# Performance work log

Measured on AMD Instinct MI355X. Metric: run time of the kernel, lower is better.

## Reference

```python
import jax, jax.numpy as jnp
import numpy as np

N_NODES = 100000
N_EDGES = 1600000
IN_DIM = 128
HID = 128
OUT_DIM = 64
N_GRAPHS = 128
BN_EPS = 1e-5


def _bn(h, gamma, beta):
    # training-mode BatchNorm1d: biased batch statistics over the node axis
    mu = jnp.mean(h, axis=0)
    var = jnp.mean(jnp.square(h - mu), axis=0)
    return gamma * (h - mu) * jax.lax.rsqrt(var + BN_EPS) + beta


def _gcn(h, W, b, src, dst, norm, n):
    # GCNConv: x @ W, symmetric-normalized scatter-add aggregation, + bias
    h = h @ W                                   # [N, F_out]
    msg = h[src] * norm[:, None]                # gather per edge (incl. self-loops)
    agg = jax.ops.segment_sum(msg, dst, num_segments=n)
    return agg + b


def setup_inputs() -> dict:
    key = jax.random.key(0)
    ks = jax.random.split(key, 24)
    x = jax.random.normal(ks[0], (N_NODES, IN_DIM), dtype=jnp.float32)
    edge_index = jax.random.randint(ks[1], (2, N_EDGES), 0, N_NODES, dtype=jnp.int32)
    batch = jnp.sort(jax.random.randint(ks[2], (N_NODES,), 0, N_GRAPHS, dtype=jnp.int32))
    dims = [(IN_DIM, HID), (HID, HID), (HID, HID), (HID, OUT_DIM)]
    inp = {"x": x, "edge_index": edge_index, "batch": batch}
    for i, (fi, fo) in enumerate(dims):
        inp[f"W{i}"] = jax.random.normal(ks[3 + i], (fi, fo), dtype=jnp.float32) / np.sqrt(fi)
        inp[f"b{i}"] = jnp.zeros((fo,), dtype=jnp.float32)
        inp[f"g{i}"] = jnp.ones((fo,), dtype=jnp.float32)
        inp[f"be{i}"] = jnp.zeros((fo,), dtype=jnp.float32)
    inp["skip_weight"] = jnp.float32(0.1)
    return inp


def reference(x, edge_index, batch,
              W0, b0, g0, be0, W1, b1, g1, be1,
              W2, b2, g2, be2, W3, b3, g3, be3, skip_weight):
    n = x.shape[0]
    loops = jnp.arange(n, dtype=edge_index.dtype)
    src = jnp.concatenate([edge_index[0], loops])
    dst = jnp.concatenate([edge_index[1], loops])
    deg = jax.ops.segment_sum(jnp.ones_like(src, dtype=x.dtype), dst, num_segments=n)
    dinv = jax.lax.rsqrt(jnp.maximum(deg, 1.0))  # deg >= 1 due to self-loops
    norm = dinv[src] * dinv[dst]

    # layer 0 (dropout is identity in eval reference)
    h = jax.nn.relu(_bn(_gcn(x, W0, b0, src, dst, norm, n), g0, be0))
    # middle layers with skip connections
    for W, b, g, be in ((W1, b1, g1, be1), (W2, b2, g2, be2)):
        h_prev = h
        h = jax.nn.relu(_bn(_gcn(h, W, b, src, dst, norm, n), g, be))
        h = h + skip_weight * h_prev
    # final layer, no relu
    h = _bn(_gcn(h, W3, b3, src, dst, norm, n), g3, be3)

    # global mean pool over graphs
    sums = jax.ops.segment_sum(h, batch, num_segments=N_GRAPHS)
    cnts = jax.ops.segment_sum(jnp.ones((n,), dtype=h.dtype), batch, num_segments=N_GRAPHS)
    return sums / jnp.maximum(cnts, 1.0)[:, None]
```

## Files before the change

### kernel.cpp

```cpp
#include <hip/hip_runtime.h>


typedef unsigned short u16;
typedef unsigned int u32;
typedef __attribute__((ext_vector_type(8))) short bf16x8;
typedef __attribute__((ext_vector_type(4))) float f32x4;

__device__ __forceinline__ float bflo(u32 u) { return __uint_as_float(u << 16); }
__device__ __forceinline__ float bfhi(u32 u) { return __uint_as_float(u & 0xffff0000u); }
__device__ __forceinline__ u16 f2bf(float f) {
    u32 u = __float_as_uint(f);
    u32 r = u + 0x7fffu + ((u >> 16) & 1u);
    return (u16)(r >> 16);
}
__device__ __forceinline__ u32 pack2(float a, float b) {
    return (u32)f2bf(a) | ((u32)f2bf(b) << 16);
}


__global__ void k_deg(const int* __restrict__ edst, int E, int* __restrict__ deg) {
    int e = blockIdx.x * blockDim.x + threadIdx.x;
    if (e < E) atomicAdd(&deg[edst[e]], 1);
}

__global__ void k_dinv(const int* __restrict__ deg, int n, float* __restrict__ dinv) {
    int i = blockIdx.x * blockDim.x + threadIdx.x;
    if (i < n) {
        int c = deg[i] + 1;
        dinv[i] = rsqrtf((float)c);
    }
}

__global__ void k_bsum(const int* __restrict__ deg, int n, int* __restrict__ bsum) {
    __shared__ int sd[256];
    int base = blockIdx.x * 1024;
    int end = base + 1024; if (end > n) end = n;
    int s = 0;
    for (int i = base + threadIdx.x; i < end; i += 256) s += deg[i] + 1;
    sd[threadIdx.x] = s;
    __syncthreads();
    for (int off = 128; off > 0; off >>= 1) {
        if (threadIdx.x < off) sd[threadIdx.x] += sd[threadIdx.x + off];
        __syncthreads();
    }
    if (threadIdx.x == 0) bsum[blockIdx.x] = sd[0];
}

__global__ void k_scanb(int* __restrict__ bsum, int B) {
    int run = 0;
    for (int i = 0; i < B; ++i) { int v = bsum[i]; bsum[i] = run; run += v; }
}

__global__ void k_offs(const int* __restrict__ deg, int n, const int* __restrict__ bsum,
                       int* __restrict__ offs) {
    __shared__ int sd[256];
    int base = blockIdx.x * 1024;
    int carry = bsum[blockIdx.x];
    for (int tile = 0; tile < 4; ++tile) {
        int i = base + tile * 256 + threadIdx.x;
        int v = (i < n) ? (deg[i] + 1) : 0;
        sd[threadIdx.x] = v;
        __syncthreads();
        int x = v;
        for (int off = 1; off < 256; off <<= 1) {
            int y = (threadIdx.x >= off) ? sd[threadIdx.x - off] : 0;
            __syncthreads();
            x += y;
            sd[threadIdx.x] = x;
            __syncthreads();
        }
        if (i < n) offs[i] = carry + x - v;
        if (i == n - 1) offs[n] = carry + x;
        carry += sd[255];
        __syncthreads();
    }
}

__global__ void k_fill_edges(const int* __restrict__ esrc, const int* __restrict__ edst, int E,
                             const float* __restrict__ dinv, const int* __restrict__ offs,
                             int* __restrict__ cursor, uint2* __restrict__ csre) {
    int e = blockIdx.x * blockDim.x + threadIdx.x;
    if (e < E) {
        int s = esrc[e], d = edst[e];
        int slot = offs[d] + atomicAdd(&cursor[d], 1);
        csre[slot] = make_uint2((u32)s, __float_as_uint(dinv[s] * dinv[d]));
    }
}

__global__ void k_fill_self(int n, const float* __restrict__ dinv, const int* __restrict__ offs,
                            int* __restrict__ cursor, uint2* __restrict__ csre) {
    int i = blockIdx.x * blockDim.x + threadIdx.x;
    if (i < n) {
        int slot = offs[i] + atomicAdd(&cursor[i], 1);
        csre[slot] = make_uint2((u32)i, __float_as_uint(dinv[i] * dinv[i]));
    }
}

__global__ void k_gcnt_bs(const int* __restrict__ batch, int n, int* __restrict__ gcnt) {
    int g = threadIdx.x;
    if (g < 128) {
        int lo0 = 0, hi0 = n;
        while (lo0 < hi0) { int m = (lo0 + hi0) >> 1; if (batch[m] < g) lo0 = m + 1; else hi0 = m; }
        int lo1 = lo0, hi1 = n;
        while (lo1 < hi1) { int m = (lo1 + hi1) >> 1; if (batch[m] < g + 1) lo1 = m + 1; else hi1 = m; }
        gcnt[g] = lo1 - lo0;
    }
}


template <int FOUT>
__global__ void k_wt(const float* __restrict__ W, u16* __restrict__ Wt) {
    __shared__ u16 l[128 * (FOUT + 8)];
    for (int i = threadIdx.x; i < 128 * FOUT; i += 256) {
        int k = i / FOUT, nn = i % FOUT;
        l[k * (FOUT + 8) + nn] = f2bf(W[i]);
    }
    __syncthreads();
    for (int i = threadIdx.x; i < 128 * FOUT; i += 256) {
        int nn = i >> 7, k = i & 127;
        Wt[nn * 128 + k] = l[k * (FOUT + 8) + nn];
    }
}


template <int FOUT, int MODE, bool STOREH>
__global__ __launch_bounds__(256) void k_gemm_mfma(const void* __restrict__ Ap,
                                                   const u16* __restrict__ hprev,
                                                   const float* __restrict__ coef,
                                                   const float* __restrict__ swp,
                                                   const u16* __restrict__ Wt,
                                                   u16* __restrict__ hout,
                                                   u16* __restrict__ O, int n) {
    constexpr int NT = FOUT / 16;
    const int lane = threadIdx.x & 63;
    const int wave = threadIdx.x >> 6;
    const int fr = lane & 15;
    const int fq = lane >> 4;
    const int rowbase = blockIdx.x * 64 + wave * 16;
    const int arow = rowbase + fr;
    const bool aok = arow < n;
    const float* af = (const float*)Ap + (size_t)arow * 128 + fq * 8;
    const u16* hp = (MODE == 3) ? hprev + (size_t)arow * 128 + fq * 8 : nullptr;
    const u16* wp = Wt + fr * 128 + fq * 8;
    float sw = 0.f;
    if constexpr (MODE == 3) sw = *swp;

    f32x4 acc[NT];
#pragma unroll
    for (int t = 0; t < NT; ++t)
#pragma unroll
        for (int q = 0; q < 4; ++q) acc[t][q] = 0.f;

#pragma unroll
    for (int kk = 0; kk < 4; ++kk) {
        bf16x8 a;
#pragma unroll
        for (int q = 0; q < 8; ++q) a[q] = 0;
        if (aok) {
            if constexpr (MODE == 1) {
                const float4 x0 = *(const float4*)(af + kk * 32);
                const float4 x1 = *(const float4*)(af + kk * 32 + 4);
                a[0] = (short)f2bf(x0.x); a[1] = (short)f2bf(x0.y);
                a[2] = (short)f2bf(x0.z); a[3] = (short)f2bf(x0.w);
                a[4] = (short)f2bf(x1.x); a[5] = (short)f2bf(x1.y);
                a[6] = (short)f2bf(x1.z); a[7] = (short)f2bf(x1.w);
            } else {
                const int k0 = kk * 32 + fq * 8;
                const float4 v0 = *(const float4*)(af + kk * 32);
                const float4 v1 = *(const float4*)(af + kk * 32 + 4);
                const float4 sc0 = *(const float4*)&coef[k0];
                const float4 sc1 = *(const float4*)&coef[k0 + 4];
                const float4 sh0 = *(const float4*)&coef[128 + k0];
                const float4 sh1 = *(const float4*)&coef[128 + k0 + 4];
                float r[8];
                r[0] = fmaxf(fmaf(v0.x, sc0.x, sh0.x), 0.f);
                r[1] = fmaxf(fmaf(v0.y, sc0.y, sh0.y), 0.f);
                r[2] = fmaxf(fmaf(v0.z, sc0.z, sh0.z), 0.f);
                r[3] = fmaxf(fmaf(v0.w, sc0.w, sh0.w), 0.f);
                r[4] = fmaxf(fmaf(v1.x, sc1.x, sh1.x), 0.f);
                r[5] = fmaxf(fmaf(v1.y, sc1.y, sh1.y), 0.f);
                r[6] = fmaxf(fmaf(v1.z, sc1.z, sh1.z), 0.f);
                r[7] = fmaxf(fmaf(v1.w, sc1.w, sh1.w), 0.f);
                if constexpr (MODE == 3) {
                    const uint4 pv = *(const uint4*)(hp + kk * 32);
                    r[0] = fmaf(sw, bflo(pv.x), r[0]); r[1] = fmaf(sw, bfhi(pv.x), r[1]);
                    r[2] = fmaf(sw, bflo(pv.y), r[2]); r[3] = fmaf(sw, bfhi(pv.y), r[3]);
                    r[4] = fmaf(sw, bflo(pv.z), r[4]); r[5] = fmaf(sw, bfhi(pv.z), r[5]);
                    r[6] = fmaf(sw, bflo(pv.w), r[6]); r[7] = fmaf(sw, bfhi(pv.w), r[7]);
                }
                uint4 o;
                o.x = pack2(r[0], r[1]);
                o.y = pack2(r[2], r[3]);
                o.z = pack2(r[4], r[5]);
                o.w = pack2(r[6], r[7]);
                a = *(const bf16x8*)&o;
                if constexpr (STOREH)
                    *(uint4*)&hout[(size_t)arow * 128 + k0] = o;
            }
        }
#pragma unroll
        for (int t = 0; t < NT; ++t) {
            bf16x8 b = *(const bf16x8*)(wp + t * 16 * 128 + kk * 32);
            acc[t] = __builtin_amdgcn_mfma_f32_16x16x32_bf16(a, b, acc[t], 0, 0, 0);
        }
    }
#pragma unroll
    for (int i = 0; i < 4; ++i) {
        const int row = rowbase + fq * 4 + i;
        if (row < n) {
#pragma unroll
            for (int t = 0; t < NT; ++t)
                O[(size_t)row * FOUT + t * 16 + fr] = f2bf(acc[t][i]);
        }
    }
}


template <int F>
__global__ __launch_bounds__(256) void k_agg(const u16* __restrict__ hW,
                                             const uint2* __restrict__ csre,
                                             const int* __restrict__ offs,
                                             float* __restrict__ agg, int n) {
    constexpr int TPN = F / 8;
    constexpr int NPB = 256 / TPN;
    const int lane = threadIdx.x % TPN;
    const int sub = threadIdx.x / TPN;
    const int fbase = lane * 8;

    for (int node = blockIdx.x * NPB + sub; node < n; node += gridDim.x * NPB) {
        const int beg = offs[node];
        const int end = offs[node + 1];
        float4 b0 = make_float4(0.f, 0.f, 0.f, 0.f);
        float4 b1 = make_float4(0.f, 0.f, 0.f, 0.f);
        float4 c0 = make_float4(0.f, 0.f, 0.f, 0.f);
        float4 c1 = make_float4(0.f, 0.f, 0.f, 0.f);
        int j = beg;
        for (; j + 8 <= end; j += 8) {
            uint2 ei[8];
#pragma unroll
            for (int q = 0; q < 8; ++q) ei[q] = csre[j + q];
            uint4 v[8];
#pragma unroll
            for (int q = 0; q < 8; ++q)
                v[q] = *(const uint4*)&hW[(size_t)ei[q].x * F + fbase];
#pragma unroll
            for (int q = 0; q < 8; ++q) {
                const float w = __uint_as_float(ei[q].y);
                if (q & 1) {
                    c0.x = fmaf(bflo(v[q].x), w, c0.x); c0.y = fmaf(bfhi(v[q].x), w, c0.y);
                    c0.z = fmaf(bflo(v[q].y), w, c0.z); c0.w = fmaf(bfhi(v[q].y), w, c0.w);
                    c1.x = fmaf(bflo(v[q].z), w, c1.x); c1.y = fmaf(bfhi(v[q].z), w, c1.y);
                    c1.z = fmaf(bflo(v[q].w), w, c1.z); c1.w = fmaf(bfhi(v[q].w), w, c1.w);
                } else {
                    b0.x = fmaf(bflo(v[q].x), w, b0.x); b0.y = fmaf(bfhi(v[q].x), w, b0.y);
                    b0.z = fmaf(bflo(v[q].y), w, b0.z); b0.w = fmaf(bfhi(v[q].y), w, b0.w);
                    b1.x = fmaf(bflo(v[q].z), w, b1.x); b1.y = fmaf(bfhi(v[q].z), w, b1.y);
                    b1.z = fmaf(bflo(v[q].w), w, b1.z); b1.w = fmaf(bfhi(v[q].w), w, b1.w);
                }
            }
        }
        for (; j < end; ++j) {
            const uint2 e0 = csre[j];
            const float w = __uint_as_float(e0.y);
            const uint4 v0 = *(const uint4*)&hW[(size_t)e0.x * F + fbase];
            b0.x = fmaf(bflo(v0.x), w, b0.x); b0.y = fmaf(bfhi(v0.x), w, b0.y);
            b0.z = fmaf(bflo(v0.y), w, b0.z); b0.w = fmaf(bfhi(v0.y), w, b0.w);
            b1.x = fmaf(bflo(v0.z), w, b1.x); b1.y = fmaf(bfhi(v0.z), w, b1.y);
            b1.z = fmaf(bflo(v0.w), w, b1.z); b1.w = fmaf(bfhi(v0.w), w, b1.w);
        }
        b0.x += c0.x; b0.y += c0.y; b0.z += c0.z; b0.w += c0.w;
        b1.x += c1.x; b1.y += c1.y; b1.z += c1.z; b1.w += c1.w;
        __builtin_nontemporal_store(*(const f32x4*)&b0,
                                    (f32x4*)&agg[(size_t)node * F + fbase]);
        __builtin_nontemporal_store(*(const f32x4*)&b1,
                                    (f32x4*)&agg[(size_t)node * F + fbase + 4]);
    }
}


template <int F>
__global__ __launch_bounds__(256) void k_stats(const float* __restrict__ aggf,
                                               float* __restrict__ stats,
                                               int* __restrict__ ticket,
                                               const float* __restrict__ g,
                                               const float* __restrict__ be,
                                               float* __restrict__ coef,
                                               float inv_n, int n8) {
    constexpr int TPR = F / 8;
    const int tid0 = blockIdx.x * 256 + threadIdx.x;
    float s[8], q[8];
#pragma unroll
    for (int k = 0; k < 8; ++k) { s[k] = 0.f; q[k] = 0.f; }
    for (int i = tid0; i < n8; i += gridDim.x * 256) {
        const float4 v0 = *(const float4*)&aggf[(size_t)i * 8];
        const float4 v1 = *(const float4*)&aggf[(size_t)i * 8 + 4];
        s[0] += v0.x; s[1] += v0.y; s[2] += v0.z; s[3] += v0.w;
        s[4] += v1.x; s[5] += v1.y; s[6] += v1.z; s[7] += v1.w;
        q[0] = fmaf(v0.x, v0.x, q[0]); q[1] = fmaf(v0.y, v0.y, q[1]);
        q[2] = fmaf(v0.z, v0.z, q[2]); q[3] = fmaf(v0.w, v0.w, q[3]);
        q[4] = fmaf(v1.x, v1.x, q[4]); q[5] = fmaf(v1.y, v1.y, q[5]);
        q[6] = fmaf(v1.z, v1.z, q[6]); q[7] = fmaf(v1.w, v1.w, q[7]);
    }
#pragma unroll
    for (int m = TPR; m < 64; m <<= 1) {
#pragma unroll
        for (int k = 0; k < 8; ++k) {
            s[k] += __shfl_xor(s[k], m);
            q[k] += __shfl_xor(q[k], m);
        }
    }
    __shared__ float sred[2][4][TPR * 8];
    const int w = threadIdx.x >> 6;
    const int l64 = threadIdx.x & 63;
    if (l64 < TPR) {
#pragma unroll
        for (int k = 0; k < 8; ++k) {
            sred[0][w][l64 * 8 + k] = s[k];
            sred[1][w][l64 * 8 + k] = q[k];
        }
    }
    __syncthreads();
    if (threadIdx.x < TPR * 8) {
        float a = sred[0][0][threadIdx.x] + sred[0][1][threadIdx.x] +
                  sred[0][2][threadIdx.x] + sred[0][3][threadIdx.x];
        float b = sred[1][0][threadIdx.x] + sred[1][1][threadIdx.x] +
                  sred[1][2][threadIdx.x] + sred[1][3][threadIdx.x];
        const int ff = threadIdx.x & (F - 1);
        atomicAdd(&stats[ff], a);
        atomicAdd(&stats[F + ff], b);
    }
    __threadfence();
    __shared__ int last;
    if (threadIdx.x == 0) last = (atomicAdd(ticket, 1) == (int)gridDim.x - 1) ? 1 : 0;
    __syncthreads();
    if (last) {
        if (threadIdx.x < F) {
            const int f = threadIdx.x;
            float sum = atomicAdd(&stats[f], 0.f);
            float ssq = atomicAdd(&stats[F + f], 0.f);
            float mean = sum * inv_n;
            float var = fmaxf(ssq * inv_n - mean * mean, 0.f);
            float sc = g[f] * rsqrtf(var + 1e-5f);
            coef[f] = sc;
            coef[F + f] = be[f] - mean * sc;
        }
    }
}


__global__ __launch_bounds__(256) void k_bnpool(const float* __restrict__ C,
                                                const int* __restrict__ batch,
                                                const float* __restrict__ coef,
                                                float* __restrict__ out, int n,
                                                int chunk) {
    __shared__ float pool[128 * 64];
    for (int i = threadIdx.x; i < 128 * 64; i += 256) pool[i] = 0.f;
    __syncthreads();
    const int f = threadIdx.x & 63;
    const int sub = threadIdx.x >> 6;
    const float sc = coef[f];
    const float sh = coef[64 + f];
    const int lo = blockIdx.x * chunk;
    int hi = lo + chunk; if (hi > n) hi = n;
    for (int node = lo + sub; node < hi; node += 4) {
        float v = fmaf(sc, C[(size_t)node * 64 + f], sh);
        int g = batch[node];
        atomicAdd(&pool[g * 64 + f], v);
    }
    __syncthreads();
    for (int i = threadIdx.x; i < 128 * 64; i += 256) {
        float v = pool[i];
        if (v != 0.f) atomicAdd(&out[i], v);
    }
}

__global__ void k_div(float* __restrict__ out, const int* __restrict__ gcnt, int total) {
    int i = blockIdx.x * blockDim.x + threadIdx.x;
    if (i < total) {
        int g = i >> 6;
        int c = gcnt[g];
        if (c < 1) c = 1;
        out[i] = out[i] / (float)c;
    }
}


static inline size_t align256(size_t x) { return (x + 255) & ~(size_t)255; }

extern "C" void kernel_launch(void* const* d_in, const int* in_sizes, int n_in,
                              void* d_out, int out_size, void* d_ws, size_t ws_size,
                              hipStream_t stream) {
    const float* x    = (const float*)d_in[0];
    const int* ei     = (const int*)d_in[1];
    const int* batch  = (const int*)d_in[2];
    const float* W0   = (const float*)d_in[3];
    const float* g0   = (const float*)d_in[5];
    const float* be0  = (const float*)d_in[6];
    const float* W1   = (const float*)d_in[7];
    const float* g1   = (const float*)d_in[9];
    const float* be1  = (const float*)d_in[10];
    const float* W2   = (const float*)d_in[11];
    const float* g2   = (const float*)d_in[13];
    const float* be2  = (const float*)d_in[14];
    const float* W3   = (const float*)d_in[15];
    const float* g3   = (const float*)d_in[17];
    const float* be3  = (const float*)d_in[18];
    const float* swp  = (const float*)d_in[19];

    const int N = in_sizes[0] / 128;
    const int E = in_sizes[1] / 2;
    const int T = E + N;
    const int* esrc = ei;
    const int* edst = ei + E;

    char* p = (char*)d_ws;
    auto carve = [&](size_t bytes) -> char* {
        char* r = p;
        p += align256(bytes);
        return r;
    };
    int*   deg    = (int*)carve((size_t)N * 4);
    float* dinv   = (float*)carve((size_t)N * 4);
    int*   offs   = (int*)carve((size_t)(N + 1) * 4);
    int*   cursor = (int*)carve((size_t)N * 4);
    int*   bsum   = (int*)carve(256 * 4);
    uint2* csre   = (uint2*)carve((size_t)T * 8);
    float* stats  = (float*)carve(4 * 256 * 4);
    float* coef   = (float*)carve(4 * 256 * 4);
    int*   ticket = (int*)carve(4 * 4);
    int*   gcnt   = (int*)carve(128 * 4);
    u16*   Wt0    = (u16*)carve(128 * 128 * 2);
    u16*   Wt1    = (u16*)carve(128 * 128 * 2);
    u16*   Wt2    = (u16*)carve(128 * 128 * 2);
    u16*   Wt3    = (u16*)carve(64 * 128 * 2);
    u16*   h0     = (u16*)carve((size_t)N * 128 * 2);
    u16*   h1     = (u16*)carve((size_t)N * 128 * 2);
    u16*   hWb    = (u16*)carve((size_t)N * 128 * 2);
    float* aggf   = (float*)carve((size_t)N * 128 * 4);

    hipMemsetAsync(deg, 0, (size_t)N * 4, stream);
    hipMemsetAsync(cursor, 0, (size_t)N * 4, stream);
    hipMemsetAsync(stats, 0, 4 * 256 * 4, stream);
    hipMemsetAsync(ticket, 0, 4 * 4, stream);
    hipMemsetAsync(d_out, 0, (size_t)out_size * 4, stream);

    const int EB = (E + 255) / 256;
    const int NB = (N + 255) / 256;
    const int B = (N + 1023) / 1024;
    k_deg<<<EB, 256, 0, stream>>>(edst, E, deg);
    k_dinv<<<NB, 256, 0, stream>>>(deg, N, dinv);
    k_bsum<<<B, 256, 0, stream>>>(deg, N, bsum);
    k_scanb<<<1, 1, 0, stream>>>(bsum, B);
    k_offs<<<B, 256, 0, stream>>>(deg, N, bsum, offs);
    k_fill_edges<<<EB, 256, 0, stream>>>(esrc, edst, E, dinv, offs, cursor, csre);
    k_fill_self<<<NB, 256, 0, stream>>>(N, dinv, offs, cursor, csre);
    k_gcnt_bs<<<1, 128, 0, stream>>>(batch, N, gcnt);

    k_wt<128><<<1, 256, 0, stream>>>(W0, Wt0);
    k_wt<128><<<1, 256, 0, stream>>>(W1, Wt1);
    k_wt<128><<<1, 256, 0, stream>>>(W2, Wt2);
    k_wt<64><<<1, 256, 0, stream>>>(W3, Wt3);

    const float inv_n = 1.0f / (float)N;
    const int gemm_grid = (N + 63) / 64;
    const int chunk = (N + 255) / 256;
    const int n8_128 = N * 16;
    const int n8_64 = N * 8;

    k_gemm_mfma<128, 1, false><<<gemm_grid, 256, 0, stream>>>(
        (const void*)x, nullptr, nullptr, nullptr, Wt0, nullptr, hWb, N);
    k_agg<128><<<2048, 256, 0, stream>>>(hWb, csre, offs, aggf, N);
    k_stats<128><<<256, 256, 0, stream>>>(aggf, stats + 0, ticket + 0, g0, be0,
                                          coef + 0, inv_n, n8_128);
    k_gemm_mfma<128, 2, true><<<gemm_grid, 256, 0, stream>>>(
        (const void*)aggf, nullptr, coef + 0, nullptr, Wt1, h0, hWb, N);
    k_agg<128><<<2048, 256, 0, stream>>>(hWb, csre, offs, aggf, N);
    k_stats<128><<<256, 256, 0, stream>>>(aggf, stats + 256, ticket + 1, g1, be1,
                                          coef + 256, inv_n, n8_128);
    k_gemm_mfma<128, 3, true><<<gemm_grid, 256, 0, stream>>>(
        (const void*)aggf, h0, coef + 256, swp, Wt2, h1, hWb, N);
    k_agg<128><<<2048, 256, 0, stream>>>(hWb, csre, offs, aggf, N);
    k_stats<128><<<256, 256, 0, stream>>>(aggf, stats + 512, ticket + 2, g2, be2,
                                          coef + 512, inv_n, n8_128);
    k_gemm_mfma<64, 3, false><<<gemm_grid, 256, 0, stream>>>(
        (const void*)aggf, h1, coef + 512, swp, Wt3, nullptr, hWb, N);
    k_agg<64><<<2048, 256, 0, stream>>>(hWb, csre, offs, aggf, N);
    k_stats<64><<<256, 256, 0, stream>>>(aggf, stats + 768, ticket + 3, g3, be3,
                                         coef + 768, inv_n, n8_64);
    k_bnpool<<<256, 256, 0, stream>>>(aggf, batch, coef + 768, (float*)d_out, N, chunk);
    k_div<<<(out_size + 255) / 256, 256, 0, stream>>>((float*)d_out, gcnt, out_size);
}
```

Before: 777.3 us.

## Two-pass bucketed CSR build to localize edge scatter writes

Replaces the single-pass random scatter of edges into the CSR with a two-pass approach. Edges are first bucketed into groups of 8 destination nodes, then scattered from the bucketed order into the final CSR. The second pass's writes and atomics are more local, which improves cache behaviour. The cost is an extra E*8-byte buffer, a second pass over the edges, and several extra small kernels, including a serial scan.

Result: slower. 877.8 us (+12.9%).

```diff
diff --git a/kernel.cpp b/kernel.cpp
--- a/kernel.cpp
+++ b/kernel.cpp
@@ -5,6 +5,8 @@
 typedef unsigned int u32;
 typedef __attribute__((ext_vector_type(8))) short bf16x8;
 typedef __attribute__((ext_vector_type(4))) float f32x4;
+
+#define BSH 3
 
 __device__ __forceinline__ float bflo(u32 u) { return __uint_as_float(u << 16); }
 __device__ __forceinline__ float bfhi(u32 u) { return __uint_as_float(u & 0xffff0000u); }
@@ -31,12 +33,13 @@
     }
 }
 
-__global__ void k_bsum(const int* __restrict__ deg, int n, int* __restrict__ bsum) {
+template <int ADD>
+__global__ void k_bsum(const int* __restrict__ cnt, int n, int* __restrict__ bsum) {
     __shared__ int sd[256];
     int base = blockIdx.x * 1024;
     int end = base + 1024; if (end > n) end = n;
     int s = 0;
-    for (int i = base + threadIdx.x; i < end; i += 256) s += deg[i] + 1;
+    for (int i = base + threadIdx.x; i < end; i += 256) s += cnt[i] + ADD;
     sd[threadIdx.x] = s;
     __syncthreads();
     for (int off = 128; off > 0; off >>= 1) {
@@ -51,14 +54,15 @@
     for (int i = 0; i < B; ++i) { int v = bsum[i]; bsum[i] = run; run += v; }
 }
 
-__global__ void k_offs(const int* __restrict__ deg, int n, const int* __restrict__ bsum,
+template <int ADD>
+__global__ void k_offs(const int* __restrict__ cnt, int n, const int* __restrict__ bsum,
                        int* __restrict__ offs) {
     __shared__ int sd[256];
     int base = blockIdx.x * 1024;
     int carry = bsum[blockIdx.x];
     for (int tile = 0; tile < 4; ++tile) {
         int i = base + tile * 256 + threadIdx.x;
-        int v = (i < n) ? (deg[i] + 1) : 0;
+        int v = (i < n) ? (cnt[i] + ADD) : 0;
         sd[threadIdx.x] = v;
         __syncthreads();
         int x = v;
@@ -76,14 +80,39 @@
     }
 }
 
-__global__ void k_fill_edges(const int* __restrict__ esrc, const int* __restrict__ edst, int E,
-                             const float* __restrict__ dinv, const int* __restrict__ offs,
-                             int* __restrict__ cursor, uint2* __restrict__ csre) {
+__global__ void k_bhist(const int* __restrict__ deg, int n, int* __restrict__ bhist,
+                        int nbk) {
+    int b = blockIdx.x * blockDim.x + threadIdx.x;
+    if (b < nbk) {
+        int lo = b << BSH;
+        int hi = lo + (1 << BSH); if (hi > n) hi = n;
+        int s = 0;
+        for (int i = lo; i < hi; ++i) s += deg[i];
+        bhist[b] = s;
+    }
+}
+
+__global__ void k_bfill(const int* __restrict__ esrc, const int* __restrict__ edst, int E,
+                        const int* __restrict__ boffs, int* __restrict__ bcur,
+                        uint2* __restrict__ ebuf) {
     int e = blockIdx.x * blockDim.x + threadIdx.x;
     if (e < E) {
-        int s = esrc[e], d = edst[e];
+        int d = edst[e];
+        int b = d >> BSH;
+        int slot = boffs[b] + atomicAdd(&bcur[b], 1);
+        ebuf[slot] = make_uint2((u32)esrc[e], (u32)d);
+    }
+}
+
+__global__ void k_fill2(const uint2* __restrict__ ebuf, int E,
+                        const float* __restrict__ dinv, const int* __restrict__ offs,
+                        int* __restrict__ cursor, uint2* __restrict__ csre) {
+    int i = blockIdx.x * blockDim.x + threadIdx.x;
+    if (i < E) {
+        const uint2 e = ebuf[i];
+        const u32 s = e.x, d = e.y;
         int slot = offs[d] + atomicAdd(&cursor[d], 1);
-        csre[slot] = make_uint2((u32)s, __float_as_uint(dinv[s] * dinv[d]));
+        csre[slot] = make_uint2(s, __float_as_uint(dinv[s] * dinv[d]));
     }
 }
 
@@ -410,6 +439,7 @@
     const int N = in_sizes[0] / 128;
     const int E = in_sizes[1] / 2;
     const int T = E + N;
+    const int NBK = (N + (1 << BSH) - 1) >> BSH;
     const int* esrc = ei;
     const int* edst = ei + E;
 
@@ -424,6 +454,10 @@
     int*   offs   = (int*)carve((size_t)(N + 1) * 4);
     int*   cursor = (int*)carve((size_t)N * 4);
     int*   bsum   = (int*)carve(256 * 4);
+    int*   bhist  = (int*)carve((size_t)(NBK + 1) * 4);
+    int*   boffs  = (int*)carve((size_t)(NBK + 1) * 4);
+    int*   bcur   = (int*)carve((size_t)NBK * 4);
+    uint2* ebuf   = (uint2*)carve((size_t)E * 8);
     uint2* csre   = (uint2*)carve((size_t)T * 8);
     float* stats  = (float*)carve(4 * 256 * 4);
     float* coef   = (float*)carve(4 * 256 * 4);
@@ -440,6 +474,7 @@
 
     hipMemsetAsync(deg, 0, (size_t)N * 4, stream);
     hipMemsetAsync(cursor, 0, (size_t)N * 4, stream);
+    hipMemsetAsync(bcur, 0, (size_t)NBK * 4, stream);
     hipMemsetAsync(stats, 0, 4 * 256 * 4, stream);
     hipMemsetAsync(ticket, 0, 4 * 4, stream);
     hipMemsetAsync(d_out, 0, (size_t)out_size * 4, stream);
@@ -447,12 +482,18 @@
     const int EB = (E + 255) / 256;
     const int NB = (N + 255) / 256;
     const int B = (N + 1023) / 1024;
+    const int B2 = (NBK + 1023) / 1024;
     k_deg<<<EB, 256, 0, stream>>>(edst, E, deg);
     k_dinv<<<NB, 256, 0, stream>>>(deg, N, dinv);
-    k_bsum<<<B, 256, 0, stream>>>(deg, N, bsum);
+    k_bsum<1><<<B, 256, 0, stream>>>(deg, N, bsum);
     k_scanb<<<1, 1, 0, stream>>>(bsum, B);
-    k_offs<<<B, 256, 0, stream>>>(deg, N, bsum, offs);
-    k_fill_edges<<<EB, 256, 0, stream>>>(esrc, edst, E, dinv, offs, cursor, csre);
+    k_offs<1><<<B, 256, 0, stream>>>(deg, N, bsum, offs);
+    k_bhist<<<(NBK + 255) / 256, 256, 0, stream>>>(deg, N, bhist, NBK);
+    k_bsum<0><<<B2, 256, 0, stream>>>(bhist, NBK, bsum);
+    k_scanb<<<1, 1, 0, stream>>>(bsum, B2);
+    k_offs<0><<<B2, 256, 0, stream>>>(bhist, NBK, bsum, boffs);
+    k_bfill<<<EB, 256, 0, stream>>>(esrc, edst, E, boffs, bcur, ebuf);
+    k_fill2<<<EB, 256, 0, stream>>>(ebuf, E, dinv, offs, cursor, csre);
     k_fill_self<<<NB, 256, 0, stream>>>(N, dinv, offs, cursor, csre);
     k_gcnt_bs<<<1, 128, 0, stream>>>(batch, N, gcnt);
 
```

## Factor symmetric GCN normalization into GEMM epilogue and aggregation output scale

Applied to the files above, without the earlier changes.

Splits the per-edge weight dinv[s]*dinv[d] into a source-side scale applied in the GEMM epilogue and a destination-side scale applied once per node after aggregation. The CSR edge array shrinks from 8-byte (index, weight) pairs to 4-byte indices, cutting edge-list traffic and removing a multiply per gathered element in the aggregation loop. The fill kernels no longer gather dinv. Rounding changes slightly because the scaled values are rounded to bf16 before aggregation.

New measurement: 801.9 us. 1.03x slower.

```diff
diff --git a/kernel.cpp b/kernel.cpp
--- a/kernel.cpp
+++ b/kernel.cpp
@@ -76,23 +76,23 @@
     }
 }
 
-__global__ void k_fill_edges(const int* __restrict__ esrc, const int* __restrict__ edst, int E,
-                             const float* __restrict__ dinv, const int* __restrict__ offs,
-                             int* __restrict__ cursor, uint2* __restrict__ csre) {
+__global__ void k_fill_edges(const int* __restrict__ esrc, const int* __restrict__ edst,
+                             int E, const int* __restrict__ offs,
+                             int* __restrict__ cursor, int* __restrict__ csri) {
     int e = blockIdx.x * blockDim.x + threadIdx.x;
     if (e < E) {
-        int s = esrc[e], d = edst[e];
+        int d = edst[e];
         int slot = offs[d] + atomicAdd(&cursor[d], 1);
-        csre[slot] = make_uint2((u32)s, __float_as_uint(dinv[s] * dinv[d]));
-    }
-}
-
-__global__ void k_fill_self(int n, const float* __restrict__ dinv, const int* __restrict__ offs,
-                            int* __restrict__ cursor, uint2* __restrict__ csre) {
+        csri[slot] = esrc[e];
+    }
+}
+
+__global__ void k_fill_self(int n, const int* __restrict__ offs,
+                            int* __restrict__ cursor, int* __restrict__ csri) {
     int i = blockIdx.x * blockDim.x + threadIdx.x;
     if (i < n) {
         int slot = offs[i] + atomicAdd(&cursor[i], 1);
-        csre[slot] = make_uint2((u32)i, __float_as_uint(dinv[i] * dinv[i]));
+        csri[slot] = i;
     }
 }
 
@@ -129,6 +129,7 @@
                                                    const float* __restrict__ coef,
                                                    const float* __restrict__ swp,
                                                    const u16* __restrict__ Wt,
+                                                   const float* __restrict__ dinv,
                                                    u16* __restrict__ hout,
                                                    u16* __restrict__ O, int n) {
     constexpr int NT = FOUT / 16;
@@ -208,9 +209,10 @@
     for (int i = 0; i < 4; ++i) {
         const int row = rowbase + fq * 4 + i;
         if (row < n) {
+            const float dv = dinv[row];
 #pragma unroll
             for (int t = 0; t < NT; ++t)
-                O[(size_t)row * FOUT + t * 16 + fr] = f2bf(acc[t][i]);
+                O[(size_t)row * FOUT + t * 16 + fr] = f2bf(acc[t][i] * dv);
         }
     }
 }
@@ -218,8 +220,9 @@
 
 template <int F>
 __global__ __launch_bounds__(256) void k_agg(const u16* __restrict__ hW,
-                                             const uint2* __restrict__ csre,
+                                             const int* __restrict__ csri,
                                              const int* __restrict__ offs,
+                                             const float* __restrict__ dinv,
                                              float* __restrict__ agg, int n) {
     constexpr int TPN = F / 8;
     constexpr int NPB = 256 / TPN;
@@ -236,40 +239,41 @@
         float4 c1 = make_float4(0.f, 0.f, 0.f, 0.f);
         int j = beg;
         for (; j + 8 <= end; j += 8) {
-            uint2 ei[8];
-#pragma unroll
-            for (int q = 0; q < 8; ++q) ei[q] = csre[j + q];
+            int si[8];
+#pragma unroll
+            for (int q = 0; q < 8; ++q) si[q] = csri[j + q];
             uint4 v[8];
 #pragma unroll
             for (int q = 0; q < 8; ++q)
-                v[q] = *(const uint4*)&hW[(size_t)ei[q].x * F + fbase];
+                v[q] = *(const uint4*)&hW[(size_t)si[q] * F + fbase];
 #pragma unroll
             for (int q = 0; q < 8; ++q) {
-                const float w = __uint_as_float(ei[q].y);
                 if (q & 1) {
-                    c0.x = fmaf(bflo(v[q].x), w, c0.x); c0.y = fmaf(bfhi(v[q].x), w, c0.y);
-                    c0.z = fmaf(bflo(v[q].y), w, c0.z); c0.w = fmaf(bfhi(v[q].y), w, c0.w);
-                    c1.x = fmaf(bflo(v[q].z), w, c1.x); c1.y = fmaf(bfhi(v[q].z), w, c1.y);
-                    c1.z = fmaf(bflo(v[q].w), w, c1.z); c1.w = fmaf(bfhi(v[q].w), w, c1.w);
+                    c0.x += bflo(v[q].x); c0.y += bfhi(v[q].x);
+                    c0.z += bflo(v[q].y); c0.w += bfhi(v[q].y);
+                    c1.x += bflo(v[q].z); c1.y += bfhi(v[q].z);
+                    c1.z += bflo(v[q].w); c1.w += bfhi(v[q].w);
                 } else {
-                    b0.x = fmaf(bflo(v[q].x), w, b0.x); b0.y = fmaf(bfhi(v[q].x), w, b0.y);
-                    b0.z = fmaf(bflo(v[q].y), w, b0.z); b0.w = fmaf(bfhi(v[q].y), w, b0.w);
-                    b1.x = fmaf(bflo(v[q].z), w, b1.x); b1.y = fmaf(bfhi(v[q].z), w, b1.y);
-                    b1.z = fmaf(bflo(v[q].w), w, b1.z); b1.w = fmaf(bfhi(v[q].w), w, b1.w);
+                    b0.x += bflo(v[q].x); b0.y += bfhi(v[q].x);
+                    b0.z += bflo(v[q].y); b0.w += bfhi(v[q].y);
+                    b1.x += bflo(v[q].z); b1.y += bfhi(v[q].z);
+                    b1.z += bflo(v[q].w); b1.w += bfhi(v[q].w);
                 }
             }
         }
         for (; j < end; ++j) {
-            const uint2 e0 = csre[j];
-            const float w = __uint_as_float(e0.y);
-            const uint4 v0 = *(const uint4*)&hW[(size_t)e0.x * F + fbase];
-            b0.x = fmaf(bflo(v0.x), w, b0.x); b0.y = fmaf(bfhi(v0.x), w, b0.y);
-            b0.z = fmaf(bflo(v0.y), w, b0.z); b0.w = fmaf(bfhi(v0.y), w, b0.w);
-            b1.x = fmaf(bflo(v0.z), w, b1.x); b1.y = fmaf(bfhi(v0.z), w, b1.y);
-            b1.z = fmaf(bflo(v0.w), w, b1.z); b1.w = fmaf(bfhi(v0.w), w, b1.w);
-        }
-        b0.x += c0.x; b0.y += c0.y; b0.z += c0.z; b0.w += c0.w;
-        b1.x += c1.x; b1.y += c1.y; b1.z += c1.z; b1.w += c1.w;
+            const int s0 = csri[j];
+            const uint4 v0 = *(const uint4*)&hW[(size_t)s0 * F + fbase];
+            b0.x += bflo(v0.x); b0.y += bfhi(v0.x);
+            b0.z += bflo(v0.y); b0.w += bfhi(v0.y);
+            b1.x += bflo(v0.z); b1.y += bfhi(v0.z);
+            b1.z += bflo(v0.w); b1.w += bfhi(v0.w);
+        }
+        const float dv = dinv[node];
+        b0.x = (b0.x + c0.x) * dv; b0.y = (b0.y + c0.y) * dv;
+        b0.z = (b0.z + c0.z) * dv; b0.w = (b0.w + c0.w) * dv;
+        b1.x = (b1.x + c1.x) * dv; b1.y = (b1.y + c1.y) * dv;
+        b1.z = (b1.z + c1.z) * dv; b1.w = (b1.w + c1.w) * dv;
         __builtin_nontemporal_store(*(const f32x4*)&b0,
                                     (f32x4*)&agg[(size_t)node * F + fbase]);
         __builtin_nontemporal_store(*(const f32x4*)&b1,
@@ -424,7 +428,7 @@
     int*   offs   = (int*)carve((size_t)(N + 1) * 4);
     int*   cursor = (int*)carve((size_t)N * 4);
     int*   bsum   = (int*)carve(256 * 4);
-    uint2* csre   = (uint2*)carve((size_t)T * 8);
+    int*   csri   = (int*)carve((size_t)T * 4);
     float* stats  = (float*)carve(4 * 256 * 4);
     float* coef   = (float*)carve(4 * 256 * 4);
     int*   ticket = (int*)carve(4 * 4);
@@ -452,8 +456,8 @@
     k_bsum<<<B, 256, 0, stream>>>(deg, N, bsum);
     k_scanb<<<1, 1, 0, stream>>>(bsum, B);
     k_offs<<<B, 256, 0, stream>>>(deg, N, bsum, offs);
-    k_fill_edges<<<EB, 256, 0, stream>>>(esrc, edst, E, dinv, offs, cursor, csre);
-    k_fill_self<<<NB, 256, 0, stream>>>(N, dinv, offs, cursor, csre);
+    k_fill_edges<<<EB, 256, 0, stream>>>(esrc, edst, E, offs, cursor, csri);
+    k_fill_self<<<NB, 256, 0, stream>>>(N, offs, cursor, csri);
     k_gcnt_bs<<<1, 128, 0, stream>>>(batch, N, gcnt);
 
     k_wt<128><<<1, 256, 0, stream>>>(W0, Wt0);
@@ -468,23 +472,23 @@
     const int n8_64 = N * 8;
 
     k_gemm_mfma<128, 1, false><<<gemm_grid, 256, 0, stream>>>(
-        (const void*)x, nullptr, nullptr, nullptr, Wt0, nullptr, hWb, N);
-    k_agg<128><<<2048, 256, 0, stream>>>(hWb, csre, offs, aggf, N);
+        (const void*)x, nullptr, nullptr, nullptr, Wt0, dinv, nullptr, hWb, N);
+    k_agg<128><<<2048, 256, 0, stream>>>(hWb, csri, offs, dinv, aggf, N);
     k_stats<128><<<256, 256, 0, stream>>>(aggf, stats + 0, ticket + 0, g0, be0,
                                           coef + 0, inv_n, n8_128);
     k_gemm_mfma<128, 2, true><<<gemm_grid, 256, 0, stream>>>(
-        (const void*)aggf, nullptr, coef + 0, nullptr, Wt1, h0, hWb, N);
-    k_agg<128><<<2048, 256, 0, stream>>>(hWb, csre, offs, aggf, N);
+        (const void*)aggf, nullptr, coef + 0, nullptr, Wt1, dinv, h0, hWb, N);
+    k_agg<128><<<2048, 256, 0, stream>>>(hWb, csri, offs, dinv, aggf, N);
     k_stats<128><<<256, 256, 0, stream>>>(aggf, stats + 256, ticket + 1, g1, be1,
                                           coef + 256, inv_n, n8_128);
     k_gemm_mfma<128, 3, true><<<gemm_grid, 256, 0, stream>>>(
-        (const void*)aggf, h0, coef + 256, swp, Wt2, h1, hWb, N);
-    k_agg<128><<<2048, 256, 0, stream>>>(hWb, csre, offs, aggf, N);
+        (const void*)aggf, h0, coef + 256, swp, Wt2, dinv, h1, hWb, N);
+    k_agg<128><<<2048, 256, 0, stream>>>(hWb, csri, offs, dinv, aggf, N);
     k_stats<128><<<256, 256, 0, stream>>>(aggf, stats + 512, ticket + 2, g2, be2,
                                           coef + 512, inv_n, n8_128);
     k_gemm_mfma<64, 3, false><<<gemm_grid, 256, 0, stream>>>(
-        (const void*)aggf, h1, coef + 512, swp, Wt3, nullptr, hWb, N);
-    k_agg<64><<<2048, 256, 0, stream>>>(hWb, csre, offs, aggf, N);
+        (const void*)aggf, h1, coef + 512, swp, Wt3, dinv, nullptr, hWb, N);
+    k_agg<64><<<2048, 256, 0, stream>>>(hWb, csri, offs, dinv, aggf, N);
     k_stats<64><<<256, 256, 0, stream>>>(aggf, stats + 768, ticket + 3, g3, be3,
                                          coef + 768, inv_n, n8_64);
     k_bnpool<<<256, 256, 0, stream>>>(aggf, batch, coef + 768, (float*)d_out, N, chunk);
```

## Fuse BatchNorm statistics into aggregation kernel and drop CSR cursor array

Applied to the files above, without the earlier changes.

Each aggregation block now accumulates per-feature sum and sum-of-squares of its output rows in shared memory with LDS atomics. It writes one partial per block, and a small per-feature reduction kernel turns these into BN scale and shift. This removes the separate stats pass that re-read the full fp32 aggregate buffer after every layer. CSR fill now reuses the degree array as a decrementing cursor, with self-loops placed at the last slot, which removes the cursor buffer and two memsets. The cost is many contended shared-memory float atomics per node in the aggregation loop, plus a non-deterministic summation order.

Measured after the change: 1.005 ms. 29.2% more time.

```diff
diff --git a/kernel.cpp b/kernel.cpp
--- a/kernel.cpp
+++ b/kernel.cpp
@@ -76,23 +76,24 @@
     }
 }
 
-__global__ void k_fill_edges(const int* __restrict__ esrc, const int* __restrict__ edst, int E,
-                             const float* __restrict__ dinv, const int* __restrict__ offs,
-                             int* __restrict__ cursor, uint2* __restrict__ csre) {
+__global__ void k_fill_edges(const int* __restrict__ esrc, const int* __restrict__ edst,
+                             int E, const float* __restrict__ dinv,
+                             const int* __restrict__ offs, int* __restrict__ deg,
+                             uint2* __restrict__ csre) {
     int e = blockIdx.x * blockDim.x + threadIdx.x;
     if (e < E) {
         int s = esrc[e], d = edst[e];
-        int slot = offs[d] + atomicAdd(&cursor[d], 1);
-        csre[slot] = make_uint2((u32)s, __float_as_uint(dinv[s] * dinv[d]));
-    }
-}
-
-__global__ void k_fill_self(int n, const float* __restrict__ dinv, const int* __restrict__ offs,
-                            int* __restrict__ cursor, uint2* __restrict__ csre) {
+        int rank = atomicSub(&deg[d], 1) - 1;
+        csre[offs[d] + rank] = make_uint2((u32)s, __float_as_uint(dinv[s] * dinv[d]));
+    }
+}
+
+__global__ void k_fill_self(int n, const float* __restrict__ dinv,
+                            const int* __restrict__ offs, uint2* __restrict__ csre) {
     int i = blockIdx.x * blockDim.x + threadIdx.x;
     if (i < n) {
-        int slot = offs[i] + atomicAdd(&cursor[i], 1);
-        csre[slot] = make_uint2((u32)i, __float_as_uint(dinv[i] * dinv[i]));
+        float dv = dinv[i];
+        csre[offs[i + 1] - 1] = make_uint2((u32)i, __float_as_uint(dv * dv));
     }
 }
 
@@ -220,12 +221,17 @@
 __global__ __launch_bounds__(256) void k_agg(const u16* __restrict__ hW,
                                              const uint2* __restrict__ csre,
                                              const int* __restrict__ offs,
-                                             float* __restrict__ agg, int n) {
+                                             float* __restrict__ agg,
+                                             float* __restrict__ partials, int n) {
     constexpr int TPN = F / 8;
     constexpr int NPB = 256 / TPN;
     const int lane = threadIdx.x % TPN;
     const int sub = threadIdx.x / TPN;
     const int fbase = lane * 8;
+
+    __shared__ float sld[2 * F];
+    for (int i = threadIdx.x; i < 2 * F; i += 256) sld[i] = 0.f;
+    __syncthreads();
 
     for (int node = blockIdx.x * NPB + sub; node < n; node += gridDim.x * NPB) {
         const int beg = offs[node];
@@ -274,76 +280,60 @@
                                     (f32x4*)&agg[(size_t)node * F + fbase]);
         __builtin_nontemporal_store(*(const f32x4*)&b1,
                                     (f32x4*)&agg[(size_t)node * F + fbase + 4]);
-    }
+        atomicAdd(&sld[fbase + 0], b0.x);
+        atomicAdd(&sld[fbase + 1], b0.y);
+        atomicAdd(&sld[fbase + 2], b0.z);
+        atomicAdd(&sld[fbase + 3], b0.w);
+        atomicAdd(&sld[fbase + 4], b1.x);
+        atomicAdd(&sld[fbase + 5], b1.y);
+        atomicAdd(&sld[fbase + 6], b1.z);
+        atomicAdd(&sld[fbase + 7], b1.w);
+        atomicAdd(&sld[F + fbase + 0], b0.x * b0.x);
+        atomicAdd(&sld[F + fbase + 1], b0.y * b0.y);
+        atomicAdd(&sld[F + fbase + 2], b0.z * b0.z);
+        atomicAdd(&sld[F + fbase + 3], b0.w * b0.w);
+        atomicAdd(&sld[F + fbase + 4], b1.x * b1.x);
+        atomicAdd(&sld[F + fbase + 5], b1.y * b1.y);
+        atomicAdd(&sld[F + fbase + 6], b1.z * b1.z);
+        atomicAdd(&sld[F + fbase + 7], b1.w * b1.w);
+    }
+    __syncthreads();
+    for (int i = threadIdx.x; i < 2 * F; i += 256)
+        partials[(size_t)blockIdx.x * 2 * F + i] = sld[i];
 }
 
 
 template <int F>
-__global__ __launch_bounds__(256) void k_stats(const float* __restrict__ aggf,
-                                               float* __restrict__ stats,
-                                               int* __restrict__ ticket,
-                                               const float* __restrict__ g,
-                                               const float* __restrict__ be,
-                                               float* __restrict__ coef,
-                                               float inv_n, int n8) {
-    constexpr int TPR = F / 8;
-    const int tid0 = blockIdx.x * 256 + threadIdx.x;
-    float s[8], q[8];
-#pragma unroll
-    for (int k = 0; k < 8; ++k) { s[k] = 0.f; q[k] = 0.f; }
-    for (int i = tid0; i < n8; i += gridDim.x * 256) {
-        const float4 v0 = *(const float4*)&aggf[(size_t)i * 8];
-        const float4 v1 = *(const float4*)&aggf[(size_t)i * 8 + 4];
-        s[0] += v0.x; s[1] += v0.y; s[2] += v0.z; s[3] += v0.w;
-        s[4] += v1.x; s[5] += v1.y; s[6] += v1.z; s[7] += v1.w;
-        q[0] = fmaf(v0.x, v0.x, q[0]); q[1] = fmaf(v0.y, v0.y, q[1]);
-        q[2] = fmaf(v0.z, v0.z, q[2]); q[3] = fmaf(v0.w, v0.w, q[3]);
-        q[4] = fmaf(v1.x, v1.x, q[4]); q[5] = fmaf(v1.y, v1.y, q[5]);
-        q[6] = fmaf(v1.z, v1.z, q[6]); q[7] = fmaf(v1.w, v1.w, q[7]);
-    }
-#pragma unroll
-    for (int m = TPR; m < 64; m <<= 1) {
-#pragma unroll
-        for (int k = 0; k < 8; ++k) {
-            s[k] += __shfl_xor(s[k], m);
-            q[k] += __shfl_xor(q[k], m);
-        }
-    }
-    __shared__ float sred[2][4][TPR * 8];
-    const int w = threadIdx.x >> 6;
-    const int l64 = threadIdx.x & 63;
-    if (l64 < TPR) {
-#pragma unroll
-        for (int k = 0; k < 8; ++k) {
-            sred[0][w][l64 * 8 + k] = s[k];
-            sred[1][w][l64 * 8 + k] = q[k];
-        }
-    }
-    __syncthreads();
-    if (threadIdx.x < TPR * 8) {
-        float a = sred[0][0][threadIdx.x] + sred[0][1][threadIdx.x] +
-                  sred[0][2][threadIdx.x] + sred[0][3][threadIdx.x];
-        float b = sred[1][0][threadIdx.x] + sred[1][1][threadIdx.x] +
-                  sred[1][2][threadIdx.x] + sred[1][3][threadIdx.x];
-        const int ff = threadIdx.x & (F - 1);
-        atomicAdd(&stats[ff], a);
-        atomicAdd(&stats[F + ff], b);
-    }
-    __threadfence();
-    __shared__ int last;
-    if (threadIdx.x == 0) last = (atomicAdd(ticket, 1) == (int)gridDim.x - 1) ? 1 : 0;
-    __syncthreads();
-    if (last) {
-        if (threadIdx.x < F) {
-            const int f = threadIdx.x;
-            float sum = atomicAdd(&stats[f], 0.f);
-            float ssq = atomicAdd(&stats[F + f], 0.f);
-            float mean = sum * inv_n;
-            float var = fmaxf(ssq * inv_n - mean * mean, 0.f);
-            float sc = g[f] * rsqrtf(var + 1e-5f);
-            coef[f] = sc;
-            coef[F + f] = be[f] - mean * sc;
-        }
+__global__ __launch_bounds__(256) void k_redcoef(const float* __restrict__ partials,
+                                                 const float* __restrict__ g,
+                                                 const float* __restrict__ be,
+                                                 float* __restrict__ coef,
+                                                 float inv_n, int nb) {
+    const int f = blockIdx.x;
+    float s = 0.f, q = 0.f;
+    for (int b = threadIdx.x; b < nb; b += 256) {
+        s += partials[(size_t)b * 2 * F + f];
+        q += partials[(size_t)b * 2 * F + F + f];
+    }
+#pragma unroll
+    for (int m = 1; m < 64; m <<= 1) {
+        s += __shfl_xor(s, m);
+        q += __shfl_xor(q, m);
+    }
+    __shared__ float rs[4], rq[4];
+    if ((threadIdx.x & 63) == 0) {
+        rs[threadIdx.x >> 6] = s;
+        rq[threadIdx.x >> 6] = q;
+    }
+    __syncthreads();
+    if (threadIdx.x == 0) {
+        float sum = rs[0] + rs[1] + rs[2] + rs[3];
+        float ssq = rq[0] + rq[1] + rq[2] + rq[3];
+        float mean = sum * inv_n;
+        float var = fmaxf(ssq * inv_n - mean * mean, 0.f);
+        float sc = g[f] * rsqrtf(var + 1e-5f);
+        coef[f] = sc;
+        coef[F + f] = be[f] - mean * sc;
     }
 }
 
@@ -422,12 +412,10 @@
     int*   deg    = (int*)carve((size_t)N * 4);
     float* dinv   = (float*)carve((size_t)N * 4);
     int*   offs   = (int*)carve((size_t)(N + 1) * 4);
-    int*   cursor = (int*)carve((size_t)N * 4);
     int*   bsum   = (int*)carve(256 * 4);
     uint2* csre   = (uint2*)carve((size_t)T * 8);
-    float* stats  = (float*)carve(4 * 256 * 4);
+    float* partials = (float*)carve((size_t)2048 * 256 * 4);
     float* coef   = (float*)carve(4 * 256 * 4);
-    int*   ticket = (int*)carve(4 * 4);
     int*   gcnt   = (int*)carve(128 * 4);
     u16*   Wt0    = (u16*)carve(128 * 128 * 2);
     u16*   Wt1    = (u16*)carve(128 * 128 * 2);
@@ -439,9 +427,6 @@
     float* aggf   = (float*)carve((size_t)N * 128 * 4);
 
     hipMemsetAsync(deg, 0, (size_t)N * 4, stream);
-    hipMemsetAsync(cursor, 0, (size_t)N * 4, stream);
-    hipMemsetAsync(stats, 0, 4 * 256 * 4, stream);
-    hipMemsetAsync(ticket, 0, 4 * 4, stream);
     hipMemsetAsync(d_out, 0, (size_t)out_size * 4, stream);
 
     const int EB = (E + 255) / 256;
@@ -452,8 +437,8 @@
     k_bsum<<<B, 256, 0, stream>>>(deg, N, bsum);
     k_scanb<<<1, 1, 0, stream>>>(bsum, B);
     k_offs<<<B, 256, 0, stream>>>(deg, N, bsum, offs);
-    k_fill_edges<<<EB, 256, 0, stream>>>(esrc, edst, E, dinv, offs, cursor, csre);
-    k_fill_self<<<NB, 256, 0, stream>>>(N, dinv, offs, cursor, csre);
+    k_fill_self<<<NB, 256, 0, stream>>>(N, dinv, offs, csre);
+    k_fill_edges<<<EB, 256, 0, stream>>>(esrc, edst, E, dinv, offs, deg, csre);
     k_gcnt_bs<<<1, 128, 0, stream>>>(batch, N, gcnt);
 
     k_wt<128><<<1, 256, 0, stream>>>(W0, Wt0);
@@ -464,29 +449,24 @@
     const float inv_n = 1.0f / (float)N;
     const int gemm_grid = (N + 63) / 64;
     const int chunk = (N + 255) / 256;
-    const int n8_128 = N * 16;
-    const int n8_64 = N * 8;
+    const int AG = 2048;
 
     k_gemm_mfma<128, 1, false><<<gemm_grid, 256, 0, stream>>>(
         (const void*)x, nullptr, nullptr, nullptr, Wt0, nullptr, hWb, N);
-    k_agg<128><<<2048, 256, 0, stream>>>(hWb, csre, offs, aggf, N);
-    k_stats<128><<<256, 256, 0, stream>>>(aggf, stats + 0, ticket + 0, g0, be0,
-                                          coef + 0, inv_n, n8_128);
+    k_agg<128><<<AG, 256, 0, stream>>>(hWb, csre, offs, aggf, partials, N);
+    k_redcoef<128><<<128, 256, 0, stream>>>(partials, g0, be0, coef + 0, inv_n, AG);
     k_gemm_mfma<128, 2, true><<<gemm_grid, 256, 0, stream>>>(
         (const void*)aggf, nullptr, coef + 0, nullptr, Wt1, h0, hWb, N);
-    k_agg<128><<<2048, 256, 0, stream>>>(hWb, csre, offs, aggf, N);
-    k_stats<128><<<256, 256, 0, stream>>>(aggf, stats + 256, ticket + 1, g1, be1,
-                                          coef + 256, inv_n, n8_128);
+    k_agg<128><<<AG, 256, 0, stream>>>(hWb, csre, offs, aggf, partials, N);
+    k_redcoef<128><<<128, 256, 0, stream>>>(partials, g1, be1, coef + 256, inv_n, AG);
     k_gemm_mfma<128, 3, true><<<gemm_grid, 256, 0, stream>>>(
         (const void*)aggf, h0, coef + 256, swp, Wt2, h1, hWb, N);
-    k_agg<128><<<2048, 256, 0, stream>>>(hWb, csre, offs, aggf, N);
-    k_stats<128><<<256, 256, 0, stream>>>(aggf, stats + 512, ticket + 2, g2, be2,
-                                          coef + 512, inv_n, n8_128);
+    k_agg<128><<<AG, 256, 0, stream>>>(hWb, csre, offs, aggf, partials, N);
+    k_redcoef<128><<<128, 256, 0, stream>>>(partials, g2, be2, coef + 512, inv_n, AG);
     k_gemm_mfma<64, 3, false><<<gemm_grid, 256, 0, stream>>>(
         (const void*)aggf, h1, coef + 512, swp, Wt3, nullptr, hWb, N);
-    k_agg<64><<<2048, 256, 0, stream>>>(hWb, csre, offs, aggf, N);
-    k_stats<64><<<256, 256, 0, stream>>>(aggf, stats + 768, ticket + 3, g3, be3,
-                                         coef + 768, inv_n, n8_64);
+    k_agg<64><<<AG, 256, 0, stream>>>(hWb, csre, offs, aggf, partials, N);
+    k_redcoef<64><<<64, 256, 0, stream>>>(partials, g3, be3, coef + 768, inv_n, AG);
     k_bnpool<<<256, 256, 0, stream>>>(aggf, batch, coef + 768, (float*)d_out, N, chunk);
     k_div<<<(out_size + 255) / 256, 256, 0, stream>>>((float*)d_out, gcnt, out_size);
 }
```
